# Kernel tuning notes

Hardware: AMD Instinct MI355X
Metric: run time of the kernel (lower is better)

The kernel has to match this reference:

```python
import jax, jax.numpy as jnp
import numpy as np

N = 50000      # nodes
E = 800000     # edges (before self loops)
FE = 256       # expression features
FC = 128       # CNV features
H = 128        # hidden_channels
NC = 8         # num_classes
C = 512        # number of central nodes


def setup_inputs() -> dict:
    key = jax.random.key(0)
    ks = jax.random.split(key, 24)

    def lin(k, fi, fo):
        k1, k2 = jax.random.split(k)
        s = 1.0 / np.sqrt(fi)
        W = jax.random.uniform(k1, (fi, fo), jnp.float32, -s, s)
        b = jax.random.uniform(k2, (fo,), jnp.float32, -s, s)
        return W, b

    x = jax.random.normal(ks[0], (N, FE), jnp.float32)
    c = jax.random.normal(ks[1], (N, FC), jnp.float32)
    edge_index = jax.random.randint(ks[2], (2, E), 0, N, jnp.int32)
    central_idx = jax.random.randint(ks[3], (C,), 0, N, jnp.int32)

    W1e, b1e = lin(ks[4], FE, H)
    W2e, b2e = lin(ks[5], H, H)
    W1c, b1c = lin(ks[6], FC, H)
    W2c, b2c = lin(ks[7], H, H)
    Wm, bm = lin(ks[8], 2 * H, NC)
    Wp1, bp1 = lin(ks[9], NC, H)
    Wp2, bp2 = lin(ks[10], H, NC)

    return dict(
        x=x, c=c, edge_index=edge_index, central_idx=central_idx,
        me_x=jax.random.normal(ks[11], (FE,), jnp.float32),
        me_c=jax.random.normal(ks[12], (FC,), jnp.float32),
        W1e=W1e, b1e=b1e, eps1e=jnp.float32(0.0),
        W2e=W2e, b2e=b2e, eps2e=jnp.float32(0.0),
        W1c=W1c, b1c=b1c, eps1c=jnp.float32(0.0),
        W2c=W2c, b2c=b2c, eps2c=jnp.float32(0.0),
        Wm=Wm, bm=bm, Wp1=Wp1, bp1=bp1, Wp2=Wp2, bp2=bp2,
    )


def _gin_conv(h, src, dst, eps, W, b):
    # GINConv with nn = Linear: lin((1+eps)*x + sum_{j in N(i)} x_j)
    agg = jax.ops.segment_sum(h[src], dst, num_segments=N)  # scatter-add of messages
    return ((1.0 + eps) * h + agg) @ W + b


def reference(x, c, edge_index, central_idx, me_x, me_c,
              W1e, b1e, eps1e, W2e, b2e, eps2e,
              W1c, b1c, eps1c, W2c, b2c, eps2c,
              Wm, bm, Wp1, bp1, Wp2, bp2):
    lrelu = lambda v: jax.nn.leaky_relu(v, 0.2)

    # add self loops
    loops = jnp.arange(N, dtype=edge_index.dtype)
    src = jnp.concatenate([edge_index[0], loops])
    dst = jnp.concatenate([edge_index[1], loops])

    # replace exact-zero entries with learned missing embeddings (broadcast per row)
    x = jnp.where(x == 0, me_x[None, :], x)
    c = jnp.where(c == 0, me_c[None, :], c)

    x_exp = lrelu(_gin_conv(x, src, dst, eps1e, W1e, b1e))
    x_exp = lrelu(_gin_conv(x_exp, src, dst, eps2e, W2e, b2e))

    x_cnv = lrelu(_gin_conv(c, src, dst, eps1c, W1c, b1c))
    x_cnv = lrelu(_gin_conv(x_cnv, src, dst, eps2c, W2c, b2c))

    h = jnp.concatenate([x_exp, x_cnv], axis=1)          # [N, 2H]
    out = lrelu(h @ Wm + bm)                             # [N, NC]

    central = out[central_idx]                           # [C, NC]
    logits = jax.nn.relu(central @ Wp1 + bp1) @ Wp2 + bp2
    return out, logits
```

## Files before the change

### kernel.cpp

```cpp
#include <hip/hip_runtime.h>

typedef unsigned short u16;
typedef __attribute__((ext_vector_type(8))) short short8;
typedef __attribute__((ext_vector_type(4))) float floatx4;
typedef __attribute__((ext_vector_type(2))) float floatx2;

__device__ __forceinline__ float b2f(unsigned int ubits) {
  union { unsigned int i; float f; } cv; cv.i = ubits << 16; return cv.f;
}
__device__ __forceinline__ float hi2f(unsigned int u) {
  union { unsigned int i; float f; } cv; cv.i = u & 0xffff0000u; return cv.f;
}
__device__ __forceinline__ float lo2f(unsigned int u) {
  union { unsigned int i; float f; } cv; cv.i = u << 16; return cv.f;
}
__device__ __forceinline__ u16 f2b(float f) {
  unsigned int u = __builtin_bit_cast(unsigned int, f);
  u += 0x7fffu + ((u >> 16) & 1u);
  return (u16)(u >> 16);
}
__device__ __forceinline__ float lrelu(float v) { return v > 0.f ? v : 0.2f * v; }
__device__ __forceinline__ float rdf(bool isbf, const void* p, int idx) {
  return isbf ? b2f((unsigned int)((const u16*)p)[idx]) : ((const float*)p)[idx];
}
__device__ __forceinline__ floatx2 up2(unsigned int u) {
  return (floatx2){lo2f(u), hi2f(u)};
}

__global__ __launch_bounds__(256) void init_kernel(int* __restrict__ deg, int n,
                                                   const u16* __restrict__ probe,
                                                   int* __restrict__ flag,
                                                   int* __restrict__ colarr, int E) {
  int i0 = (blockIdx.x * 256 + threadIdx.x) * 4;
  if (i0 + 3 < n) {
    *(int4*)(deg + i0) = make_int4(0, 0, 0, 0);
  } else {
    for (int j = 0; j < 4; j++) if (i0 + j < n) deg[i0 + j] = 0;
  }
  if (blockIdx.x == 0) {
    if (threadIdx.x >= 64 && threadIdx.x < 80) colarr[E + (int)threadIdx.x - 64] = 0;
    if (threadIdx.x < 64) {
      int lane = threadIdx.x;
      int cnt = 0;
      for (int i = lane; i < 256; i += 64) {
        unsigned int u = probe[i];
        unsigned int e = (u >> 7) & 0xFFu;
        if ((u & 0x7fffu) == 0 || (e >= 60 && e <= 191)) cnt++;
      }
#pragma unroll
      for (int off = 32; off; off >>= 1) cnt += __shfl_down(cnt, off, 64);
      if (lane == 0) *flag = (cnt >= 240) ? 1 : 0;
    }
  }
}

__global__ __launch_bounds__(256) void hist_kernel(const int* __restrict__ dst, int E,
                                                   int* __restrict__ deg) {
  int i = blockIdx.x * 256 + threadIdx.x;
  if (i < E) atomicAdd(deg + dst[i], 1);
}

#define SCB 1024

__global__ __launch_bounds__(256) void scan_phaseA(const int* __restrict__ deg,
                                                   int* __restrict__ bsum, int n) {
  int i0 = blockIdx.x * SCB + threadIdx.x * 4;
  int s = 0;
  if (i0 + 3 < n) {
    int4 v = *(const int4*)(deg + i0);
    s = v.x + v.y + v.z + v.w;
  } else {
    for (int j = 0; j < 4; j++) if (i0 + j < n) s += deg[i0 + j];
  }
#pragma unroll
  for (int off = 32; off; off >>= 1) s += __shfl_down(s, off, 64);
  __shared__ int ws4[4];
  int lane = threadIdx.x & 63, wid = threadIdx.x >> 6;
  if (lane == 0) ws4[wid] = s;
  __syncthreads();
  if (threadIdx.x == 0) bsum[blockIdx.x] = ws4[0] + ws4[1] + ws4[2] + ws4[3];
}

__global__ void scan_phaseB(const int* __restrict__ bsum, int* __restrict__ boff,
                            int PB, int* __restrict__ rowptr, int n) {
  int lane = threadIdx.x;
  int v = (lane < PB) ? bsum[lane] : 0;
  int incl = v;
#pragma unroll
  for (int off = 1; off < 64; off <<= 1) {
    int t = __shfl_up(incl, off, 64);
    if (lane >= off) incl += t;
  }
  if (lane < PB) boff[lane] = incl - v;
  if (lane == 63) rowptr[n] = incl;
}

__global__ __launch_bounds__(256) void scan_phaseC(const int* __restrict__ deg,
                                                   const int* __restrict__ boff,
                                                   int* __restrict__ rowptr,
                                                   int* __restrict__ cursor, int n) {
  int i0 = blockIdx.x * SCB + threadIdx.x * 4;
  int v0 = 0, v1 = 0, v2 = 0, v3 = 0;
  if (i0 + 3 < n) {
    int4 v = *(const int4*)(deg + i0);
    v0 = v.x; v1 = v.y; v2 = v.z; v3 = v.w;
  } else {
    if (i0 < n) v0 = deg[i0];
    if (i0 + 1 < n) v1 = deg[i0 + 1];
    if (i0 + 2 < n) v2 = deg[i0 + 2];
    if (i0 + 3 < n) v3 = deg[i0 + 3];
  }
  int local = v0 + v1 + v2 + v3;
  int lane = threadIdx.x & 63, wid = threadIdx.x >> 6;
  int incl = local;
#pragma unroll
  for (int off = 1; off < 64; off <<= 1) {
    int t = __shfl_up(incl, off, 64);
    if (lane >= off) incl += t;
  }
  __shared__ int ws4[4];
  if (lane == 63) ws4[wid] = incl;
  __syncthreads();
  int woff = 0;
  for (int w = 0; w < wid; w++) woff += ws4[w];
  int run = boff[blockIdx.x] + woff + incl - local;
  if (i0 < n)     { rowptr[i0] = run;     cursor[i0] = run; }     run += v0;
  if (i0 + 1 < n) { rowptr[i0 + 1] = run; cursor[i0 + 1] = run; } run += v1;
  if (i0 + 2 < n) { rowptr[i0 + 2] = run; cursor[i0 + 2] = run; } run += v2;
  if (i0 + 3 < n) { rowptr[i0 + 3] = run; cursor[i0 + 3] = run; }
}

__global__ __launch_bounds__(256) void fill_kernel(const int* __restrict__ src,
                                                   const int* __restrict__ dst, int E,
                                                   int* __restrict__ cursor,
                                                   int* __restrict__ colarr) {
  int i = blockIdx.x * 256 + threadIdx.x;
  if (i < E) {
    int p = atomicAdd(cursor + dst[i], 1);
    colarr[p] = src[i];
  }
}

struct TWDesc {
  const void* W[5];
  int K[5];
  int Nc[5];
  int base[6];
};

__global__ __launch_bounds__(256) void transpose_all(TWDesc d, u16* __restrict__ out,
                                                     const int* __restrict__ flagp) {
  bool isbf = (*flagp != 0);
  int idx = blockIdx.x * 256 + threadIdx.x;
  if (idx >= d.base[5]) return;
  int s = 0;
  while (idx >= d.base[s + 1]) s++;
  int local = idx - d.base[s];
  int K = d.K[s], Nc = d.Nc[s];
  int nn = local / K;
  int k = local - nn * K;
  out[idx] = (nn < Nc) ? f2b(rdf(isbf, d.W[s], k * Nc + nn)) : (u16)0;
}

__device__ __forceinline__ short8 load_a_me(const void* Av, int lda, const void* me,
                                            int r, int k0, int q, bool isbf) {
  short8 a;
  if (isbf) {
    a = *(const short8*)((const u16*)Av + (long)r * lda + k0 + q * 8);
#pragma unroll
    for (int j = 0; j < 8; j++) {
      if (((u16)a[j] & 0x7fffu) == 0)
        a[j] = (short)((const u16*)me)[k0 + q * 8 + j];
    }
  } else {
    const float* A = (const float*)Av;
    const uint4* p = (const uint4*)(A + (long)r * lda + k0 + q * 8);
    uint4 w0 = p[0];
    uint4 w1 = p[1];
    unsigned int ww[8] = {w0.x, w0.y, w0.z, w0.w, w1.x, w1.y, w1.z, w1.w};
#pragma unroll
    for (int j = 0; j < 8; j++) {
      if ((ww[j] & 0x7fffffffu) == 0)
        a[j] = (short)f2b(((const float*)me)[k0 + q * 8 + j]);
      else
        a[j] = (short)f2b(__builtin_bit_cast(float, ww[j]));
    }
  }
  return a;
}

__global__ __launch_bounds__(256) void gemm_l1(
    const void* __restrict__ x, const void* __restrict__ cc,
    const void* __restrict__ mex, const void* __restrict__ mec,
    const u16* __restrict__ w1e_t, const u16* __restrict__ w1c_t,
    int M, int gb, u16* __restrict__ tb, const int* __restrict__ flagp) {
  bool isbf = (*flagp != 0);
  bool isC = (blockIdx.x >= (unsigned)gb);
  int bid = isC ? (int)blockIdx.x - gb : (int)blockIdx.x;
  int wid = threadIdx.x >> 6;
  int lane = threadIdx.x & 63;
  int l15 = lane & 15;
  int q = lane >> 4;
  int row0 = bid * 64 + wid * 16;
  int r = row0 + l15;
  if (r >= M) r = M - 1;

  const void* A  = isC ? cc : x;
  const void* me = isC ? mec : mex;
  const u16* wt  = isC ? w1c_t : w1e_t;
  int K    = isC ? 128 : 256;
  int cofs = isC ? 128 : 0;

  floatx4 acc[8];
#pragma unroll
  for (int n = 0; n < 8; n++) acc[n] = (floatx4){0, 0, 0, 0};

  for (int k0 = 0; k0 < K; k0 += 32) {
    short8 a = load_a_me(A, K, me, r, k0, q, isbf);
#pragma unroll
    for (int n = 0; n < 8; n++) {
      short8 b = *(const short8*)(wt + (n * 16 + l15) * K + k0 + q * 8);
      acc[n] = __builtin_amdgcn_mfma_f32_16x16x32_bf16(a, b, acc[n], 0, 0, 0);
    }
  }
#pragma unroll
  for (int n = 0; n < 8; n++)
#pragma unroll
    for (int rr = 0; rr < 4; rr++) {
      int row = row0 + q * 4 + rr;
      if (row < M) tb[(long)row * 256 + cofs + n * 16 + l15] = f2b(acc[n][rr]);
    }
}

__global__ __launch_bounds__(256) void gemm_l2(
    const u16* __restrict__ u,
    const u16* __restrict__ w2e_t, const u16* __restrict__ w2c_t,
    int M, int gb, u16* __restrict__ tb) {
  bool isC = (blockIdx.x >= (unsigned)gb);
  int bid = isC ? (int)blockIdx.x - gb : (int)blockIdx.x;
  int wid = threadIdx.x >> 6;
  int lane = threadIdx.x & 63;
  int l15 = lane & 15;
  int q = lane >> 4;
  int row0 = bid * 64 + wid * 16;
  int r = row0 + l15;
  if (r >= M) r = M - 1;

  const u16* wt = isC ? w2c_t : w2e_t;
  int aofs = isC ? 128 : 0;

  floatx4 acc[8];
#pragma unroll
  for (int n = 0; n < 8; n++) acc[n] = (floatx4){0, 0, 0, 0};

  for (int k0 = 0; k0 < 128; k0 += 32) {
    short8 a = *(const short8*)(u + (long)r * 256 + aofs + k0 + q * 8);
#pragma unroll
    for (int n = 0; n < 8; n++) {
      short8 b = *(const short8*)(wt + (n * 16 + l15) * 128 + k0 + q * 8);
      acc[n] = __builtin_amdgcn_mfma_f32_16x16x32_bf16(a, b, acc[n], 0, 0, 0);
    }
  }
#pragma unroll
  for (int n = 0; n < 8; n++)
#pragma unroll
    for (int rr = 0; rr < 4; rr++) {
      int row = row0 + q * 4 + rr;
      if (row < M) tb[(long)row * 256 + aofs + n * 16 + l15] = f2b(acc[n][rr]);
    }
}

__device__ __forceinline__ void gin_gather8(
    const u16* __restrict__ t, const int* __restrict__ rowptr,
    const int* __restrict__ colarr, const u16* __restrict__ zrow,
    int node, long fbB, floatx2& s01, floatx2& s23) {
  const char* base = (const char*)t + fbB;
  const char* zb = (const char*)zrow + fbB;
  s01 = (floatx2){0.f, 0.f};
  s23 = (floatx2){0.f, 0.f};
  int eu  = __builtin_amdgcn_readfirstlane(rowptr[node]);
  int e1u = __builtin_amdgcn_readfirstlane(rowptr[node + 1]);
  int c0 = colarr[eu],     c1 = colarr[eu + 1], c2 = colarr[eu + 2], c3 = colarr[eu + 3];
  int c4 = colarr[eu + 4], c5 = colarr[eu + 5], c6 = colarr[eu + 6], c7 = colarr[eu + 7];
  int eb = eu;
  for (; eb + 8 <= e1u; eb += 8) {
    uint2 w0 = *(const uint2*)(base + ((long)c0 << 9));
    uint2 w1 = *(const uint2*)(base + ((long)c1 << 9));
    uint2 w2 = *(const uint2*)(base + ((long)c2 << 9));
    uint2 w3 = *(const uint2*)(base + ((long)c3 << 9));
    uint2 w4 = *(const uint2*)(base + ((long)c4 << 9));
    uint2 w5 = *(const uint2*)(base + ((long)c5 << 9));
    uint2 w6 = *(const uint2*)(base + ((long)c6 << 9));
    uint2 w7 = *(const uint2*)(base + ((long)c7 << 9));
    int n0 = colarr[eb + 8],  n1 = colarr[eb + 9],  n2 = colarr[eb + 10], n3 = colarr[eb + 11];
    int n4 = colarr[eb + 12], n5 = colarr[eb + 13], n6 = colarr[eb + 14], n7 = colarr[eb + 15];
    s01 += up2(w0.x); s23 += up2(w0.y);
    s01 += up2(w1.x); s23 += up2(w1.y);
    s01 += up2(w2.x); s23 += up2(w2.y);
    s01 += up2(w3.x); s23 += up2(w3.y);
    s01 += up2(w4.x); s23 += up2(w4.y);
    s01 += up2(w5.x); s23 += up2(w5.y);
    s01 += up2(w6.x); s23 += up2(w6.y);
    s01 += up2(w7.x); s23 += up2(w7.y);
    c0 = n0; c1 = n1; c2 = n2; c3 = n3;
    c4 = n4; c5 = n5; c6 = n6; c7 = n7;
  }
  int rem = e1u - eb;
  if (rem > 0) {
    const char* p0 = base + ((long)c0 << 9);
    const char* p1 = (1 < rem) ? base + ((long)c1 << 9) : zb;
    const char* p2 = (2 < rem) ? base + ((long)c2 << 9) : zb;
    const char* p3 = (3 < rem) ? base + ((long)c3 << 9) : zb;
    const char* p4 = (4 < rem) ? base + ((long)c4 << 9) : zb;
    const char* p5 = (5 < rem) ? base + ((long)c5 << 9) : zb;
    const char* p6 = (6 < rem) ? base + ((long)c6 << 9) : zb;
    const char* p7 = (7 < rem) ? base + ((long)c7 << 9) : zb;
    uint2 w0 = *(const uint2*)p0;
    uint2 w1 = *(const uint2*)p1;
    uint2 w2 = *(const uint2*)p2;
    uint2 w3 = *(const uint2*)p3;
    uint2 w4 = *(const uint2*)p4;
    uint2 w5 = *(const uint2*)p5;
    uint2 w6 = *(const uint2*)p6;
    uint2 w7 = *(const uint2*)p7;
    s01 += up2(w0.x); s23 += up2(w0.y);
    s01 += up2(w1.x); s23 += up2(w1.y);
    s01 += up2(w2.x); s23 += up2(w2.y);
    s01 += up2(w3.x); s23 += up2(w3.y);
    s01 += up2(w4.x); s23 += up2(w4.y);
    s01 += up2(w5.x); s23 += up2(w5.y);
    s01 += up2(w6.x); s23 += up2(w6.y);
    s01 += up2(w7.x); s23 += up2(w7.y);
  }
}

__global__ __launch_bounds__(256) void agg_kernel(
    const u16* __restrict__ t, const int* __restrict__ rowptr, const int* __restrict__ colarr,
    const void* __restrict__ epsE, const void* __restrict__ epsC,
    const void* __restrict__ bE, const void* __restrict__ bC,
    u16* __restrict__ u, int N, const u16* __restrict__ zrow,
    const int* __restrict__ flagp) {
  int node = blockIdx.x * 4 + __builtin_amdgcn_readfirstlane(threadIdx.x >> 6);
  if (node >= N) return;
  bool isbf = (*flagp != 0);
  int lane = threadIdx.x & 63;
  int f0 = lane << 2;
  long fbB = (long)f0 << 1;
  const u16* tb = t + f0;

  uint2 ps = *(const uint2*)(tb + ((long)node << 8));

  floatx2 s01, s23;
  gin_gather8(t, rowptr, colarr, zrow, node, fbB, s01, s23);

  bool isE = (lane < 32);
  float eps2 = 2.0f + rdf(isbf, isE ? epsE : epsC, 0);
  const void* bp = isE ? bE : bC;
  int bi = isE ? f0 : (f0 - 128);
  float a0 = lrelu(s01.x + eps2 * lo2f(ps.x) + rdf(isbf, bp, bi + 0));
  float a1 = lrelu(s01.y + eps2 * hi2f(ps.x) + rdf(isbf, bp, bi + 1));
  float a2 = lrelu(s23.x + eps2 * lo2f(ps.y) + rdf(isbf, bp, bi + 2));
  float a3 = lrelu(s23.y + eps2 * hi2f(ps.y) + rdf(isbf, bp, bi + 3));
  uint2 o;
  o.x = ((unsigned int)f2b(a1) << 16) | f2b(a0);
  o.y = ((unsigned int)f2b(a3) << 16) | f2b(a2);
  *(uint2*)(u + ((long)node << 8) + f0) = o;
}

__global__ __launch_bounds__(256) void agg_head(
    const u16* __restrict__ t, const int* __restrict__ rowptr, const int* __restrict__ colarr,
    const void* __restrict__ epsE, const void* __restrict__ epsC,
    const void* __restrict__ bE, const void* __restrict__ bC,
    const u16* __restrict__ wm_t, const void* __restrict__ bm,
    float* __restrict__ out, int N, const u16* __restrict__ zrow,
    const int* __restrict__ flagp) {
  __shared__ float wmf[2048];
  __shared__ float bmf[8];
  bool isbf = (*flagp != 0);
  int tid = threadIdx.x;
  for (int i = tid; i < 2048; i += 256) wmf[i] = b2f((unsigned int)wm_t[i]);
  if (tid < 8) bmf[tid] = rdf(isbf, bm, tid);
  __syncthreads();

  int node = blockIdx.x * 4 + __builtin_amdgcn_readfirstlane(tid >> 6);
  if (node >= N) return;
  int lane = tid & 63;
  int f0 = lane << 2;
  long fbB = (long)f0 << 1;
  const u16* tb = t + f0;

  uint2 ps = *(const uint2*)(tb + ((long)node << 8));

  floatx2 s01, s23;
  gin_gather8(t, rowptr, colarr, zrow, node, fbB, s01, s23);

  bool isE = (lane < 32);
  float eps2 = 2.0f + rdf(isbf, isE ? epsE : epsC, 0);
  const void* bp = isE ? bE : bC;
  int bi = isE ? f0 : (f0 - 128);
  float a0 = lrelu(s01.x + eps2 * lo2f(ps.x) + rdf(isbf, bp, bi + 0));
  float a1 = lrelu(s01.y + eps2 * hi2f(ps.x) + rdf(isbf, bp, bi + 1));
  float a2 = lrelu(s23.x + eps2 * lo2f(ps.y) + rdf(isbf, bp, bi + 2));
  float a3 = lrelu(s23.y + eps2 * hi2f(ps.y) + rdf(isbf, bp, bi + 3));

  float p[8];
#pragma unroll
  for (int col = 0; col < 8; col++) {
    float4 w = *(const float4*)&wmf[col * 256 + f0];
    p[col] = a0 * w.x + a1 * w.y + a2 * w.z + a3 * w.w;
  }
#pragma unroll
  for (int m = 1; m < 64; m <<= 1) {
#pragma unroll
    for (int col = 0; col < 8; col++) p[col] += __shfl_xor(p[col], m, 64);
  }
  if (lane == 0) {
    float4 o0, o1;
    o0.x = lrelu(p[0] + bmf[0]); o0.y = lrelu(p[1] + bmf[1]);
    o0.z = lrelu(p[2] + bmf[2]); o0.w = lrelu(p[3] + bmf[3]);
    o1.x = lrelu(p[4] + bmf[4]); o1.y = lrelu(p[5] + bmf[5]);
    o1.z = lrelu(p[6] + bmf[6]); o1.w = lrelu(p[7] + bmf[7]);
    *(float4*)(out + (long)node * 8) = o0;
    *(float4*)(out + (long)node * 8 + 4) = o1;
  }
}

__global__ __launch_bounds__(128) void mlp_kernel(
    const float* __restrict__ outbuf, const int* __restrict__ central,
    const void* __restrict__ Wp1, const void* __restrict__ bp1,
    const void* __restrict__ Wp2, const void* __restrict__ bp2,
    float* __restrict__ logits, const int* __restrict__ flagp) {
  __shared__ float h1[128];
  __shared__ float o[8];
  bool isbf = (*flagp != 0);
  int b = blockIdx.x, tid = threadIdx.x;
  int node = central[b];
  if (tid < 8) o[tid] = outbuf[node * 8 + tid];
  __syncthreads();
  float s = rdf(isbf, bp1, tid);
#pragma unroll
  for (int k = 0; k < 8; k++) s += o[k] * rdf(isbf, Wp1, k * 128 + tid);
  h1[tid] = fmaxf(s, 0.f);
  __syncthreads();
  if (tid < 8) {
    float s2 = rdf(isbf, bp2, tid);
    for (int k = 0; k < 128; k++) s2 += h1[k] * rdf(isbf, Wp2, k * 8 + tid);
    logits[b * 8 + tid] = s2;
  }
}

extern "C" void kernel_launch(void* const* d_in, const int* in_sizes, int n_in,
                              void* d_out, int out_size, void* d_ws, size_t ws_size,
                              hipStream_t stream) {
  const void* x    = d_in[0];
  const void* c    = d_in[1];
  const int* eidx  = (const int*)d_in[2];
  const int* cidx  = (const int*)d_in[3];
  const void* me_x = d_in[4];
  const void* me_c = d_in[5];
  const void* W1e  = d_in[6];
  const void* b1e  = d_in[7];
  const void* e1e  = d_in[8];
  const void* W2e  = d_in[9];
  const void* b2e  = d_in[10];
  const void* e2e  = d_in[11];
  const void* W1c  = d_in[12];
  const void* b1c  = d_in[13];
  const void* e1c  = d_in[14];
  const void* W2c  = d_in[15];
  const void* b2c  = d_in[16];
  const void* e2c  = d_in[17];
  const void* Wm   = d_in[18];
  const void* bm   = d_in[19];
  const void* Wp1  = d_in[20];
  const void* bp1  = d_in[21];
  const void* Wp2  = d_in[22];
  const void* bp2  = d_in[23];

  const int N = in_sizes[0] / 256;
  const int E = in_sizes[2] / 2;
  const int Cn = in_sizes[3];
  const int* src = eidx;
  const int* dst = eidx + E;

  char* ws = (char*)d_ws;
  int* deg    = (int*)(ws + 0);
  int* rowptr = (int*)(ws + 200192);
  int* cursor = (int*)(ws + 400384);
  int* colarr = (int*)(ws + 600576);
  u16* tbuf   = (u16*)(ws + 3800832);
  u16* ubuf   = (u16*)(ws + 29400832);
  u16* wt_all = (u16*)(ws + 55000832);
  int* flag   = (int*)(ws + 55172864);
  int* bsum   = (int*)(ws + 55173120);
  int* boff   = (int*)(ws + 55173376);

  u16* w1e_t = wt_all + 0;
  u16* w1c_t = wt_all + 32768;
  u16* w2e_t = wt_all + 49152;
  u16* w2c_t = wt_all + 65536;
  u16* wm_t  = wt_all + 81920;
  const u16* zrow = wt_all + 83968;

  init_kernel<<<(N + 1023) / 1024, 256, 0, stream>>>(deg, N, (const u16*)x, flag,
                                                     colarr, E);

  hist_kernel<<<(E + 255) / 256, 256, 0, stream>>>(dst, E, deg);
  int PB = (N + SCB - 1) / SCB;
  scan_phaseA<<<PB, 256, 0, stream>>>(deg, bsum, N);
  scan_phaseB<<<1, 64, 0, stream>>>(bsum, boff, PB, rowptr, N);
  scan_phaseC<<<PB, 256, 0, stream>>>(deg, boff, rowptr, cursor, N);
  fill_kernel<<<(E + 255) / 256, 256, 0, stream>>>(src, dst, E, cursor, colarr);

  TWDesc td;
  td.W[0] = W1e; td.K[0] = 256; td.Nc[0] = 128;
  td.W[1] = W1c; td.K[1] = 128; td.Nc[1] = 128;
  td.W[2] = W2e; td.K[2] = 128; td.Nc[2] = 128;
  td.W[3] = W2c; td.K[3] = 128; td.Nc[3] = 128;
  td.W[4] = Wm;  td.K[4] = 256; td.Nc[4] = 8;
  td.base[0] = 0; td.base[1] = 32768; td.base[2] = 49152;
  td.base[3] = 65536; td.base[4] = 81920; td.base[5] = 86016;
  transpose_all<<<(86016 + 255) / 256, 256, 0, stream>>>(td, wt_all, flag);

  int gb = (N + 63) / 64;
  gemm_l1<<<2 * gb, 256, 0, stream>>>(x, c, me_x, me_c, w1e_t, w1c_t, N, gb, tbuf, flag);
  agg_kernel<<<(N + 3) / 4, 256, 0, stream>>>(tbuf, rowptr, colarr,
      e1e, e1c, b1e, b1c, ubuf, N, zrow, flag);
  gemm_l2<<<2 * gb, 256, 0, stream>>>(ubuf, w2e_t, w2c_t, N, gb, tbuf);
  agg_head<<<(N + 3) / 4, 256, 0, stream>>>(tbuf, rowptr, colarr,
      e2e, e2c, b2e, b2c, wm_t, bm, (float*)d_out, N, zrow, flag);
  mlp_kernel<<<Cn, 128, 0, stream>>>((const float*)d_out, cidx,
      Wp1, bp1, Wp2, bp2, (float*)d_out + (size_t)N * 8, flag);
}
```

Measured before the change: 440.4 us.

## Stage transposed weights in LDS with k8-major layout for layer GEMMs

The weight transpose now writes the four 128-column weight matrices in a k-chunk-major layout (8 k values per column contiguous, grouped by 8-wide k blocks). Both layer GEMM kernels copy the whole weight matrix into shared memory once per block with 16-byte loads and then read B fragments from LDS instead of global memory. This removes repeated global/L2 weight fetches per block. In exchange it adds a per-block preload and barrier, and uses up to 64KB of LDS, which limits occupancy.

```diff
diff --git a/kernel.cpp b/kernel.cpp
--- a/kernel.cpp
+++ b/kernel.cpp
@@ -156,10 +156,18 @@
   int s = 0;
   while (idx >= d.base[s + 1]) s++;
   int local = idx - d.base[s];
-  int K = d.K[s], Nc = d.Nc[s];
-  int nn = local / K;
-  int k = local - nn * K;
-  out[idx] = (nn < Nc) ? f2b(rdf(isbf, d.W[s], k * Nc + nn)) : (u16)0;
+  if (s < 4) {
+    int k8 = local >> 10;
+    int rem = local & 1023;
+    int col = rem >> 3;
+    int k7 = rem & 7;
+    int k = k8 * 8 + k7;
+    out[idx] = f2b(rdf(isbf, d.W[s], k * 128 + col));
+  } else {
+    int nn = local >> 8;
+    int k = local & 255;
+    out[idx] = (nn < d.Nc[4]) ? f2b(rdf(isbf, d.W[4], k * d.Nc[4] + nn)) : (u16)0;
+  }
 }
 
 __device__ __forceinline__ short8 load_a_me(const void* Av, int lda, const void* me,
@@ -194,11 +202,13 @@
     const void* __restrict__ mex, const void* __restrict__ mec,
     const u16* __restrict__ w1e_t, const u16* __restrict__ w1c_t,
     int M, int gb, u16* __restrict__ tb, const int* __restrict__ flagp) {
+  __shared__ __align__(16) u16 bs[32768];
   bool isbf = (*flagp != 0);
   bool isC = (blockIdx.x >= (unsigned)gb);
   int bid = isC ? (int)blockIdx.x - gb : (int)blockIdx.x;
-  int wid = threadIdx.x >> 6;
-  int lane = threadIdx.x & 63;
+  int tid = threadIdx.x;
+  int wid = tid >> 6;
+  int lane = tid & 63;
   int l15 = lane & 15;
   int q = lane >> 4;
   int row0 = bid * 64 + wid * 16;
@@ -211,15 +221,21 @@
   int K    = isC ? 128 : 256;
   int cofs = isC ? 128 : 0;
 
+  int nchunk = K * 16;
+  for (int i = tid; i < nchunk; i += 256)
+    *(uint4*)(bs + i * 8) = *(const uint4*)(wt + i * 8);
+  __syncthreads();
+
   floatx4 acc[8];
 #pragma unroll
   for (int n = 0; n < 8; n++) acc[n] = (floatx4){0, 0, 0, 0};
 
   for (int k0 = 0; k0 < K; k0 += 32) {
     short8 a = load_a_me(A, K, me, r, k0, q, isbf);
+    const u16* bb = bs + ((k0 >> 3) + q) * 1024 + l15 * 8;
 #pragma unroll
     for (int n = 0; n < 8; n++) {
-      short8 b = *(const short8*)(wt + (n * 16 + l15) * K + k0 + q * 8);
+      short8 b = *(const short8*)(bb + n * 128);
       acc[n] = __builtin_amdgcn_mfma_f32_16x16x32_bf16(a, b, acc[n], 0, 0, 0);
     }
   }
@@ -236,10 +252,12 @@
     const u16* __restrict__ u,
     const u16* __restrict__ w2e_t, const u16* __restrict__ w2c_t,
     int M, int gb, u16* __restrict__ tb) {
+  __shared__ __align__(16) u16 bs[16384];
   bool isC = (blockIdx.x >= (unsigned)gb);
   int bid = isC ? (int)blockIdx.x - gb : (int)blockIdx.x;
-  int wid = threadIdx.x >> 6;
-  int lane = threadIdx.x & 63;
+  int tid = threadIdx.x;
+  int wid = tid >> 6;
+  int lane = tid & 63;
   int l15 = lane & 15;
   int q = lane >> 4;
   int row0 = bid * 64 + wid * 16;
@@ -249,15 +267,20 @@
   const u16* wt = isC ? w2c_t : w2e_t;
   int aofs = isC ? 128 : 0;
 
+  for (int i = tid; i < 2048; i += 256)
+    *(uint4*)(bs + i * 8) = *(const uint4*)(wt + i * 8);
+  __syncthreads();
+
   floatx4 acc[8];
 #pragma unroll
   for (int n = 0; n < 8; n++) acc[n] = (floatx4){0, 0, 0, 0};
 
   for (int k0 = 0; k0 < 128; k0 += 32) {
     short8 a = *(const short8*)(u + (long)r * 256 + aofs + k0 + q * 8);
+    const u16* bb = bs + ((k0 >> 3) + q) * 1024 + l15 * 8;
 #pragma unroll
     for (int n = 0; n < 8; n++) {
-      short8 b = *(const short8*)(wt + (n * 16 + l15) * 128 + k0 + q * 8);
+      short8 b = *(const short8*)(bb + n * 128);
       acc[n] = __builtin_amdgcn_mfma_f32_16x16x32_bf16(a, b, acc[n], 0, 0, 0);
     }
   }
```

New measurement: 419.1 us. -4.8%, faster.
